# Performance work log

Measured on AMD Instinct MI355X. Metric: run time of the kernel, lower is better.

The kernel has to match this reference:

```python
import jax, jax.numpy as jnp
import numpy as np

GAMMA = 2.0
POS_RATIO = 0.7
MARGIN = 100.0
TOPK = 10


def setup_inputs() -> dict:
    key = jax.random.key(0)
    k1, k2, k3, k4, k5 = jax.random.split(key, 5)
    N, C = 64, 256
    Hg = Wg = 14
    Hl = Wl = 10
    gl_sa_maps = jax.random.normal(k1, (2 * N, C, Hg, Wg), dtype=jnp.float32)
    lo_sa_maps = jax.random.normal(k2, (6 * N, C, Hl, Wl), dtype=jnp.float32)
    gl_projs_ng = jax.random.normal(k3, (2 * N, C, Hg, Wg), dtype=jnp.float32)
    # valid crop boxes: (x0, y0, x1, y1) with x1 > x0, y1 > y0, all in [0, 1]
    starts = jax.random.uniform(k4, (8, N, 2), minval=0.0, maxval=0.4)
    sizes = jax.random.uniform(k5, (8, N, 2), minval=0.4, maxval=0.6)
    coords = jnp.concatenate([starts, starts + sizes], axis=-1).astype(jnp.float32)
    return {"gl_sa_maps": gl_sa_maps, "lo_sa_maps": lo_sa_maps,
            "gl_projs_ng": gl_projs_ng, "coords": coords}


def _centers(coord, H, W):
    # coord: [N, 4] = (x0, y0, x1, y1)
    bw = (coord[:, 2] - coord[:, 0]) / W  # [N]
    bh = (coord[:, 3] - coord[:, 1]) / H
    yy, xx = jnp.meshgrid(jnp.arange(H, dtype=coord.dtype),
                          jnp.arange(W, dtype=coord.dtype), indexing="ij")
    # flattened row-major (x fastest), matching the torch view/reshape order
    cx = (xx.reshape(-1)[None, :] + 0.5) * bw[:, None] + coord[:, 0:1]  # [N, HW]
    cy = (yy.reshape(-1)[None, :] + 0.5) * bh[:, None] + coord[:, 1:2]
    diag = jnp.sqrt(bw ** 2 + bh ** 2)  # [N]
    return cx, cy, diag


def _regression_loss(q, k, coord_q, coord_k):
    N, C, Hq, Wq = q.shape
    _, _, Hk, Wk = k.shape
    qf = q.reshape(N, C, Hq * Wq)
    kf = k.reshape(N, C, Hk * Wk)
    cqx, cqy, qd = _centers(coord_q, Hq, Wq)
    ckx, cky, kd = _centers(coord_k, Hk, Wk)
    max_diag = jnp.maximum(qd, kd)[:, None, None]
    dist = jnp.sqrt((cqx[:, :, None] - ckx[:, None, :]) ** 2
                    + (cqy[:, :, None] - cky[:, None, :]) ** 2) / max_diag
    pos_mask = jax.lax.stop_gradient((dist < POS_RATIO).astype(q.dtype))  # [N, HqWq, HkWk]
    logits = -2.0 * jnp.einsum("ncq,nck->nqk", qf, kf)
    positives = (logits * pos_mask).sum((-2, -1)) / (pos_mask.sum((-2, -1)) + 1e-6)
    masked = jnp.where(pos_mask > 0, jnp.inf, logits)
    # smallest TOPK, sorted ascending (matches torch.topk largest=False)
    small = -jax.lax.top_k(-masked, TOPK)[0]  # [N, HqWq, TOPK]
    negatives = small[:, :, 1:].mean(-1).mean(-1)  # [N]
    # MarginRankingLoss(margin)(negatives, gamma*positives, y=1)
    return jnp.mean(jnp.maximum(0.0, -(negatives - GAMMA * positives) + MARGIN))


def reference(gl_sa_maps, lo_sa_maps, gl_projs_ng, coords):
    gl_sa = jnp.split(gl_sa_maps, 2)
    gl_pr = jnp.split(gl_projs_ng, 2)
    lo_sa = jnp.split(lo_sa_maps, 6)
    gl_coords = coords[:2]
    lo_coords = coords[2:]
    loss = jnp.float32(0.0)
    n_terms = 0
    for j in range(2):
        for i in range(2):
            if i == j:
                continue
            loss = loss + _regression_loss(gl_sa[i], gl_pr[j], gl_coords[i], gl_coords[j])
            n_terms += 1
        for i in range(6):
            loss = loss + _regression_loss(lo_sa[i], gl_pr[j], lo_coords[i], gl_coords[j])
            n_terms += 1
    return loss / n_terms
```

## Files before the change

kernel.cpp:

```cpp
#include <hip/hip_runtime.h>

#define NN 64
#define B_PER_MAT (8 * 14 * 64)
#define B_OFF 0
#define PART_OFF_F (128 * B_PER_MAT * 4)

typedef __attribute__((ext_vector_type(8))) short short8;
typedef __attribute__((ext_vector_type(4))) float f32x4;

__device__ __forceinline__ float waveSum(float v) {
#pragma unroll
  for (int m = 1; m < 64; m <<= 1) v += __shfl_xor(v, m, 64);
  return v;
}

__device__ __forceinline__ float rowMin16(float v) {
  int x = __builtin_bit_cast(int, v);
  v = fminf(v, __builtin_bit_cast(float, __builtin_amdgcn_update_dpp(x, x, 0xB1, 0xF, 0xF, true)));
  x = __builtin_bit_cast(int, v);
  v = fminf(v, __builtin_bit_cast(float, __builtin_amdgcn_update_dpp(x, x, 0x4E, 0xF, 0xF, true)));
  x = __builtin_bit_cast(int, v);
  v = fminf(v, __builtin_bit_cast(float, __builtin_amdgcn_update_dpp(x, x, 0x124, 0xF, 0xF, true)));
  x = __builtin_bit_cast(int, v);
  v = fminf(v, __builtin_bit_cast(float, __builtin_amdgcn_update_dpp(x, x, 0x128, 0xF, 0xF, true)));
  return v;
}

__device__ __forceinline__ unsigned short f2bf(float f) {
  unsigned u = __builtin_bit_cast(unsigned, f);
  u += 0x7FFFu + ((u >> 16) & 1u);
  return (unsigned short)(u >> 16);
}
__device__ __forceinline__ unsigned packbf(float a, float b) {
  return (unsigned)f2bf(a) | ((unsigned)f2bf(b) << 16);
}

__global__ void __launch_bounds__(256) convert_b_kernel(
    const float* __restrict__ gl_pr, uint4* __restrict__ ws) {
  const int b = blockIdx.x;
  const int m = b >> 3, kc8 = b & 7;
  const float* src = gl_pr + (size_t)m * 256 * 196 + (size_t)kc8 * 32 * 196;
  uint4* dst = ws + B_OFF + (size_t)m * B_PER_MAT + kc8 * 14 * 64;

  const int quad = threadIdx.x >> 6, colq = threadIdx.x & 63;
  if (colq >= 56) return;
  const int col0 = colq * 4;
  uint4 u0, u1, u2, u3;
  if (col0 < 196) {
    const float* p = src + (size_t)(quad * 8) * 196 + col0;
    float4 g[8];
#pragma unroll
    for (int e = 0; e < 8; ++e) g[e] = *(const float4*)(p + (size_t)e * 196);
    u0.x = packbf(g[0].x, g[1].x); u0.y = packbf(g[2].x, g[3].x);
    u0.z = packbf(g[4].x, g[5].x); u0.w = packbf(g[6].x, g[7].x);
    u1.x = packbf(g[0].y, g[1].y); u1.y = packbf(g[2].y, g[3].y);
    u1.z = packbf(g[4].y, g[5].y); u1.w = packbf(g[6].y, g[7].y);
    u2.x = packbf(g[0].z, g[1].z); u2.y = packbf(g[2].z, g[3].z);
    u2.z = packbf(g[4].z, g[5].z); u2.w = packbf(g[6].z, g[7].z);
    u3.x = packbf(g[0].w, g[1].w); u3.y = packbf(g[2].w, g[3].w);
    u3.z = packbf(g[4].w, g[5].w); u3.w = packbf(g[6].w, g[7].w);
  } else {
    u0 = u1 = u2 = u3 = make_uint4(0, 0, 0, 0);
  }
  const int tile = colq >> 2, li0 = col0 & 15;
  uint4* d = dst + (size_t)tile * 64 + quad * 16 + li0;
  d[0] = u0; d[1] = u1; d[2] = u2; d[3] = u3;
}

__global__ void __launch_bounds__(256, 4) triplet_main(
    const float* __restrict__ gl_sa, const float* __restrict__ lo_sa,
    const uint4* __restrict__ ws, const float* __restrict__ coords,
    float* __restrict__ partials) {
  __shared__ uint4 bbuf[2][14][64];
  __shared__ float red[3][4];
  const int tid = threadIdx.x;
  const int lane = tid & 63;
  const int li = lane & 15;
  const int quad = lane >> 4;
  const int w = tid >> 6;

  int b = blockIdx.x;
  int jn = b >> 4, u = b & 15;
  int j = jn >> 6, n = jn & 63;
  const uint4* bbase = ws + B_OFF + (size_t)(j * NN + n) * B_PER_MAT;
  const float *cqp, *ckp = coords + (j * NN + n) * 4;
  const float* asrc;
  int Q, Wq, ntA, rowbase;
  if (u < 4) {
    rowbase = u * 64;
    Q = 196; Wq = 14; ntA = 13;
    asrc = gl_sa + (size_t)((1 - j) * NN + n) * 256 * 196;
    cqp = coords + ((1 - j) * NN + n) * 4;
  } else {
    int v = u - 4, i = v >> 1, g = v & 1;
    rowbase = g * 64;
    Q = 100; Wq = 10; ntA = 7;
    asrc = lo_sa + (size_t)(i * NN + n) * 256 * 100;
    cqp = coords + ((2 + i) * NN + n) * 4;
  }
  const int rt = (rowbase >> 4) + w;
  const bool active = rt < ntA;
  const int arow = rt * 16 + li;
  const bool rvalid = active && (arow < Q);
  const float* agp = asrc + (size_t)(quad * 8) * Q + (rvalid ? arow : 0);

  f32x4 acc[14];
#pragma unroll
  for (int t = 0; t < 14; ++t) acc[t] = 0.0f;

#pragma unroll 1
  for (int c8 = 0; c8 < 4; ++c8) {
    uint4 a0, a1;
    if (active) {
      const float* p0 = agp + (size_t)(c8 * 64) * Q;
      const float* p1 = p0 + (size_t)32 * Q;
      float v0[8], v1[8];
#pragma unroll
      for (int e = 0; e < 8; ++e) {
        v0[e] = rvalid ? p0[(size_t)e * Q] : 0.0f;
        v1[e] = rvalid ? p1[(size_t)e * Q] : 0.0f;
      }
      a0.x = packbf(v0[0], v0[1]); a0.y = packbf(v0[2], v0[3]);
      a0.z = packbf(v0[4], v0[5]); a0.w = packbf(v0[6], v0[7]);
      a1.x = packbf(v1[0], v1[1]); a1.y = packbf(v1[2], v1[3]);
      a1.z = packbf(v1[4], v1[5]); a1.w = packbf(v1[6], v1[7]);
    }
    const uint4* bs = bbase + (size_t)c8 * (2 * 14 * 64);
#pragma unroll
    for (int it = 0; it < 7; ++it) {
      int idx = it * 256 + (w << 6);
      __builtin_amdgcn_global_load_lds(
          (const __attribute__((address_space(1))) void*)(bs + idx + lane),
          (__attribute__((address_space(3))) void*)((uint4*)bbuf + idx),
          16, 0, 0);
    }
    __syncthreads();
    if (active) {
#pragma unroll
      for (int t = 0; t < 14; ++t) {
        short8 bf = __builtin_bit_cast(short8, bbuf[0][t][lane]);
        acc[t] = __builtin_amdgcn_mfma_f32_16x16x32_bf16(
            __builtin_bit_cast(short8, a0), bf, acc[t], 0, 0, 0);
      }
#pragma unroll
      for (int t = 0; t < 14; ++t) {
        short8 bf = __builtin_bit_cast(short8, bbuf[1][t][lane]);
        acc[t] = __builtin_amdgcn_mfma_f32_16x16x32_bf16(
            __builtin_bit_cast(short8, a1), bf, acc[t], 0, 0, 0);
      }
    }
    __syncthreads();
  }

  const float qx0 = cqp[0], qy0 = cqp[1];
  const float bwq = (cqp[2] - qx0) / (float)Wq;
  const float bhq = (cqp[3] - qy0) / (float)Wq;
  const float kx0 = ckp[0], ky0 = ckp[1];
  const float bwk = (ckp[2] - kx0) / 14.0f;
  const float bhk = (ckp[3] - ky0) / 14.0f;
  const float qd = sqrtf(bwq * bwq + bhq * bhq);
  const float kd = sqrtf(bwk * bwk + bhk * bhk);
  const float md = fmaxf(qd, kd);
  const float thr2 = 0.49f * md * md;
  const float INFV = __builtin_inff();

  float ckx[14], cky[14];
  unsigned kvalid = 0;
#pragma unroll
  for (int t = 0; t < 14; ++t) {
    int col = t * 16 + li;
    if (col < 196) kvalid |= (1u << t);
    int xk = col % 14, yk = col / 14;
    ckx[t] = ((float)xk + 0.5f) * bwk + kx0;
    cky[t] = ((float)yk + 0.5f) * bhk + ky0;
  }

  const unsigned Mdiv = (Wq == 14) ? 4682u : 6554u;
  unsigned r0u = (unsigned)(rowbase + w * 16 + quad * 4);
  unsigned yq = (r0u * Mdiv) >> 16;
  unsigned xq = r0u - yq * (unsigned)Wq;

  float psum = 0.f, pcnt = 0.f, nsum = 0.f;
#pragma unroll
  for (int rg = 0; rg < 4; ++rg) {
    int r = rowbase + w * 16 + quad * 4 + rg;
    if (r < Q) {
      float cqx = ((float)xq + 0.5f) * bwq + qx0;
      float cqy = ((float)yq + 0.5f) * bhq + qy0;
      float s0v = INFV, s1v = INFV, s2v = INFV, s3v = INFV, s4v = INFV,
            rest = INFV;
#pragma unroll
      for (int t = 0; t < 14; ++t) {
        float v = -2.0f * acc[t][rg];
        float dx = cqx - ckx[t], dy = cqy - cky[t];
        float d2 = dx * dx + dy * dy;
        bool kv = (kvalid >> t) & 1;
        bool pos = kv && (d2 < thr2);
        psum += pos ? v : 0.0f;
        pcnt += pos ? 1.0f : 0.0f;
        float a = (kv && !pos) ? v : INFV;
        float mn;
        mn = fminf(a, s0v); a = fmaxf(a, s0v); s0v = mn;
        mn = fminf(a, s1v); a = fmaxf(a, s1v); s1v = mn;
        mn = fminf(a, s2v); a = fmaxf(a, s2v); s2v = mn;
        mn = fminf(a, s3v); a = fmaxf(a, s3v); s3v = mn;
        mn = fminf(a, s4v); a = fmaxf(a, s4v); s4v = mn;
        rest = fminf(rest, a);
      }
      float mm = rowMin16(s0v);
      float first = mm, total = mm;
      {
        unsigned long long bal = __ballot(s0v == mm);
        unsigned qb = (unsigned)(bal >> (quad << 4)) & 0xFFFFu;
        if (li == __ffs(qb) - 1) {
          s0v = s1v; s1v = s2v; s2v = s3v; s3v = s4v; s4v = rest; rest = INFV;
        }
      }
#pragma unroll 1
      for (int s = 1; s < 10; ++s) {
        mm = rowMin16(s0v);
        total += mm;
        unsigned long long bal = __ballot(s0v == mm);
        unsigned qb = (unsigned)(bal >> (quad << 4)) & 0xFFFFu;
        if (li == __ffs(qb) - 1) {
          s0v = s1v; s1v = s2v; s2v = s3v; s3v = s4v; s4v = rest; rest = INFV;
        }
      }
      if (li == 0) nsum += (total - first) * (1.0f / 9.0f);
    }
    xq++;
    if (xq == (unsigned)Wq) { xq = 0; yq++; }
  }

  psum = waveSum(psum);
  pcnt = waveSum(pcnt);
  nsum = waveSum(nsum);
  if (lane == 0) {
    red[0][w] = psum;
    red[1][w] = pcnt;
    red[2][w] = nsum;
  }
  __syncthreads();
  if (tid == 0) {
    float* pb = partials + (size_t)blockIdx.x * 3;
    pb[0] = red[0][0] + red[0][1] + red[0][2] + red[0][3];
    pb[1] = red[1][0] + red[1][1] + red[1][2] + red[1][3];
    pb[2] = red[2][0] + red[2][1] + red[2][2] + red[2][3];
  }
}

__global__ void __launch_bounds__(256) finalize_kernel(
    const float* __restrict__ partials, float* __restrict__ out) {
  int tid = threadIdx.x;
  float sum = 0.f;
  for (int e = tid; e < 14 * NN; e += 256) {
    float P = 0.f, C = 0.f, Ns = 0.f, Qf;
    if (e < 128) {
      int t = e >> 6, n = e & 63;
      Qf = 196.0f;
      int base = ((t * 64 + n) * 16) * 3;
#pragma unroll
      for (int g = 0; g < 4; ++g) {
        P += partials[base + 3 * g];
        C += partials[base + 3 * g + 1];
        Ns += partials[base + 3 * g + 2];
      }
    } else {
      int s = e - 128;
      int idx = s >> 6, n = s & 63;
      int j = idx / 6, i = idx - 6 * j;
      Qf = 100.0f;
      int base = ((j * 64 + n) * 16 + 4 + 2 * i) * 3;
#pragma unroll
      for (int g = 0; g < 2; ++g) {
        P += partials[base + 3 * g];
        C += partials[base + 3 * g + 1];
        Ns += partials[base + 3 * g + 2];
      }
    }
    float positives = P / (C + 1e-6f);
    float negatives = Ns / Qf;
    sum += fmaxf(0.0f, 100.0f - (negatives - 2.0f * positives));
  }
  sum = waveSum(sum);
  __shared__ float ssum[4];
  if ((tid & 63) == 0) ssum[tid >> 6] = sum;
  __syncthreads();
  if (tid == 0) out[0] = (ssum[0] + ssum[1] + ssum[2] + ssum[3]) * (1.0f / (14 * NN));
}

extern "C" void kernel_launch(void* const* d_in, const int* in_sizes, int n_in,
                              void* d_out, int out_size, void* d_ws, size_t ws_size,
                              hipStream_t stream) {
  const float* gl_sa = (const float*)d_in[0];
  const float* lo_sa = (const float*)d_in[1];
  const float* gl_pr = (const float*)d_in[2];
  const float* coords = (const float*)d_in[3];
  uint4* frags = (uint4*)d_ws;
  float* partials = (float*)d_ws + PART_OFF_F;
  float* out = (float*)d_out;

  convert_b_kernel<<<1024, 256, 0, stream>>>(gl_pr, frags);
  triplet_main<<<2048, 256, 0, stream>>>(gl_sa, lo_sa, frags, coords, partials);
  finalize_kernel<<<1, 256, 0, stream>>>(partials, out);
}
```

Before: 167.1 us.

## Unroll K loop and prefetch next A chunk during MFMAs; raise occupancy bound

The four-iteration K loop is fully unrolled with double-buffered A registers, so the strided global gather of the next A chunk is issued between the two MFMA halves of the current chunk. This hides A-load latency behind matrix math. Launch bounds move from 4 to 5 blocks per SM, which tightens the register budget and raises the risk of spills given the extra live A registers.

Result: slower. 222.6 us (+33.2%).

```diff
diff --git a/kernel.cpp b/kernel.cpp
--- a/kernel.cpp
+++ b/kernel.cpp
@@ -67,7 +67,43 @@
   d[0] = u0; d[1] = u1; d[2] = u2; d[3] = u3;
 }
 
-__global__ void __launch_bounds__(256, 4) triplet_main(
+#define GATHER_A(C8, A0, A1)                                                 \
+  if (active) {                                                              \
+    const float* p0 = agp + (size_t)((C8) * 64) * Q;                         \
+    const float* p1 = p0 + (size_t)32 * Q;                                   \
+    float v0[8], v1[8];                                                      \
+    _Pragma("unroll") for (int e = 0; e < 8; ++e) {                          \
+      v0[e] = rvalid ? p0[(size_t)e * Q] : 0.0f;                             \
+      v1[e] = rvalid ? p1[(size_t)e * Q] : 0.0f;                             \
+    }                                                                        \
+    A0.x = packbf(v0[0], v0[1]); A0.y = packbf(v0[2], v0[3]);                \
+    A0.z = packbf(v0[4], v0[5]); A0.w = packbf(v0[6], v0[7]);                \
+    A1.x = packbf(v1[0], v1[1]); A1.y = packbf(v1[2], v1[3]);                \
+    A1.z = packbf(v1[4], v1[5]); A1.w = packbf(v1[6], v1[7]);                \
+  }
+
+#define ISSUE_B(C8)                                                          \
+  {                                                                          \
+    const uint4* bs = bbase + (size_t)(C8) * (2 * 14 * 64);                  \
+    _Pragma("unroll") for (int it = 0; it < 7; ++it) {                       \
+      int idx = it * 256 + (w << 6);                                         \
+      __builtin_amdgcn_global_load_lds(                                      \
+          (const __attribute__((address_space(1))) void*)(bs + idx + lane),  \
+          (__attribute__((address_space(3))) void*)((uint4*)bbuf + idx),     \
+          16, 0, 0);                                                         \
+    }                                                                        \
+  }
+
+#define MFMA_HALF(KC, AREG)                                                  \
+  if (active) {                                                              \
+    _Pragma("unroll") for (int t = 0; t < 14; ++t) {                         \
+      short8 bf = __builtin_bit_cast(short8, bbuf[KC][t][lane]);             \
+      acc[t] = __builtin_amdgcn_mfma_f32_16x16x32_bf16(                      \
+          __builtin_bit_cast(short8, AREG), bf, acc[t], 0, 0, 0);            \
+    }                                                                        \
+  }
+
+__global__ void __launch_bounds__(256, 5) triplet_main(
     const float* __restrict__ gl_sa, const float* __restrict__ lo_sa,
     const uint4* __restrict__ ws, const float* __restrict__ coords,
     float* __restrict__ partials) {
@@ -108,49 +144,34 @@
 #pragma unroll
   for (int t = 0; t < 14; ++t) acc[t] = 0.0f;
 
-#pragma unroll 1
-  for (int c8 = 0; c8 < 4; ++c8) {
-    uint4 a0, a1;
-    if (active) {
-      const float* p0 = agp + (size_t)(c8 * 64) * Q;
-      const float* p1 = p0 + (size_t)32 * Q;
-      float v0[8], v1[8];
-#pragma unroll
-      for (int e = 0; e < 8; ++e) {
-        v0[e] = rvalid ? p0[(size_t)e * Q] : 0.0f;
-        v1[e] = rvalid ? p1[(size_t)e * Q] : 0.0f;
-      }
-      a0.x = packbf(v0[0], v0[1]); a0.y = packbf(v0[2], v0[3]);
-      a0.z = packbf(v0[4], v0[5]); a0.w = packbf(v0[6], v0[7]);
-      a1.x = packbf(v1[0], v1[1]); a1.y = packbf(v1[2], v1[3]);
-      a1.z = packbf(v1[4], v1[5]); a1.w = packbf(v1[6], v1[7]);
-    }
-    const uint4* bs = bbase + (size_t)c8 * (2 * 14 * 64);
-#pragma unroll
-    for (int it = 0; it < 7; ++it) {
-      int idx = it * 256 + (w << 6);
-      __builtin_amdgcn_global_load_lds(
-          (const __attribute__((address_space(1))) void*)(bs + idx + lane),
-          (__attribute__((address_space(3))) void*)((uint4*)bbuf + idx),
-          16, 0, 0);
-    }
-    __syncthreads();
-    if (active) {
-#pragma unroll
-      for (int t = 0; t < 14; ++t) {
-        short8 bf = __builtin_bit_cast(short8, bbuf[0][t][lane]);
-        acc[t] = __builtin_amdgcn_mfma_f32_16x16x32_bf16(
-            __builtin_bit_cast(short8, a0), bf, acc[t], 0, 0, 0);
-      }
-#pragma unroll
-      for (int t = 0; t < 14; ++t) {
-        short8 bf = __builtin_bit_cast(short8, bbuf[1][t][lane]);
-        acc[t] = __builtin_amdgcn_mfma_f32_16x16x32_bf16(
-            __builtin_bit_cast(short8, a1), bf, acc[t], 0, 0, 0);
-      }
-    }
-    __syncthreads();
-  }
+  uint4 a0A, a1A, a0B, a1B;
+  ISSUE_B(0);
+  GATHER_A(0, a0A, a1A);
+  __syncthreads();
+
+  MFMA_HALF(0, a0A);
+  GATHER_A(1, a0B, a1B);
+  MFMA_HALF(1, a1A);
+  __syncthreads();
+  ISSUE_B(1);
+  __syncthreads();
+
+  MFMA_HALF(0, a0B);
+  GATHER_A(2, a0A, a1A);
+  MFMA_HALF(1, a1B);
+  __syncthreads();
+  ISSUE_B(2);
+  __syncthreads();
+
+  MFMA_HALF(0, a0A);
+  GATHER_A(3, a0B, a1B);
+  MFMA_HALF(1, a1A);
+  __syncthreads();
+  ISSUE_B(3);
+  __syncthreads();
+
+  MFMA_HALF(0, a0B);
+  MFMA_HALF(1, a1B);
 
   const float qx0 = cqp[0], qy0 = cqp[1];
   const float bwq = (cqp[2] - qx0) / (float)Wq;
```
